# Kernel tuning notes

Hardware: AMD Instinct MI355X
Metric: run time of the kernel (lower is better)

## Reference

```python
import jax, jax.numpy as jnp
import numpy as np

B, S, D, H, F = 2, 2048, 2048, 16, 8192
HD = D // H  # 128
EPS = 1e-5


def setup_inputs() -> dict:
    key = jax.random.key(0)
    ks = jax.random.split(key, 10)
    s = 0.02
    return {
        "x": jax.random.normal(ks[0], (B, S, D), dtype=jnp.float32),
        "rms_w": jnp.ones((D,), dtype=jnp.float32),
        "w_qkv": jax.random.normal(ks[1], (3 * D, D), dtype=jnp.float32) * s,
        "w_out": jax.random.normal(ks[2], (D, D), dtype=jnp.float32) * s,
        "w1": jax.random.normal(ks[3], (F, D), dtype=jnp.float32) * s,
        "b1": jnp.zeros((F,), dtype=jnp.float32),
        "w3": jax.random.normal(ks[4], (F, D), dtype=jnp.float32) * s,
        "b3": jnp.zeros((F,), dtype=jnp.float32),
        "w2": jax.random.normal(ks[5], (D, F), dtype=jnp.float32) * s,
        "b2": jnp.zeros((D,), dtype=jnp.float32),
    }


def reference(x, rms_w, w_qkv, w_out, w1, b1, w3, b3, w2, b2):
    b, s, d = x.shape
    # RMSNorm (computed in fp32 as in original)
    xf = x.astype(jnp.float32)
    xn = (xf * jax.lax.rsqrt(jnp.mean(xf * xf, axis=-1, keepdims=True) + EPS)).astype(x.dtype) * rms_w
    # QKV projection: Linear(dim, 3*dim, bias=False) then 'b n (qkv h d) -> qkv b h n d'
    qkv = jnp.einsum('bsd,ed->bse', xn, w_qkv).reshape(b, s, 3, H, HD)
    qkv = jnp.transpose(qkv, (2, 0, 3, 1, 4))  # [3, b, h, s, hd]
    q, k, v = qkv[0], qkv[1], qkv[2]
    # Naive causal attention with explicit [b,h,s,s] score matrix
    scores = jnp.einsum('bhqd,bhkd->bhqk', q, k) / jnp.sqrt(jnp.float32(HD)).astype(x.dtype)
    causal = jnp.tril(jnp.ones((s, s), dtype=bool))
    scores = jnp.where(causal[None, None], scores, -jnp.inf)
    p = jax.nn.softmax(scores, axis=-1)
    # dropout p=0.0 -> identity
    out = jnp.einsum('bhqk,bhkd->bhqd', p, v)
    # Faithful to original: .view(bs, seqlen, h*d) on [b,h,s,hd] = raw row-major reshape
    out = out.reshape(b, s, H * HD)
    h = out @ w_out.T
    # FeedForward: w2(w1(h) + relu(w3(h))), biases per nn.Linear defaults
    ffn = ((h @ w1.T + b1) + jax.nn.relu(h @ w3.T + b3)) @ w2.T + b2
    return x + ffn
```

## Files before the change

### kernel.cpp

```cpp
#include <hip/hip_runtime.h>
#include <hip/hip_bf16.h>
#include <cstdint>

#define BB 2
#define SS 2048
#define DD 2048
#define HH 16
#define HD 128
#define FF 8192
#define QKVD 6144

typedef __bf16 bf16x8 __attribute__((ext_vector_type(8)));
typedef float floatx4 __attribute__((ext_vector_type(4)));

#define LOG2E 1.4426950408889634f

__device__ __forceinline__ unsigned short f2bf(float f) {
  unsigned u = __builtin_bit_cast(unsigned, f);
  u += 0x7FFFu + ((u >> 16) & 1u);
  return (unsigned short)(u >> 16);
}
__device__ __forceinline__ float bf2f(unsigned short h) {
  return __builtin_bit_cast(float, (unsigned)h << 16);
}

__device__ __forceinline__ void load_lds_16B(const void* g, void* l) {
  __builtin_amdgcn_global_load_lds(
      (const __attribute__((address_space(1))) unsigned int*)g,
      (__attribute__((address_space(3))) unsigned int*)l, 16, 0, 0);
}

__global__ void f32_to_bf16_vec(const float* __restrict__ src,
                                unsigned short* __restrict__ dst, int n4) {
  int i = blockIdx.x * 256 + threadIdx.x;
  if (i < n4) {
    float4 v = ((const float4*)src)[i];
    ushort4 o;
    o.x = f2bf(v.x); o.y = f2bf(v.y); o.z = f2bf(v.z); o.w = f2bf(v.w);
    ((ushort4*)dst)[i] = o;
  }
}

__global__ __launch_bounds__(256) void rmsnorm_bf16(const float* __restrict__ x,
                                                    const float* __restrict__ w,
                                                    unsigned short* __restrict__ xn) {
  const int row = blockIdx.x, tid = threadIdx.x;
  const float4* xr = (const float4*)(x + (size_t)row * DD);
  float4 a = xr[tid], b = xr[tid + 256];
  float ss = a.x * a.x + a.y * a.y + a.z * a.z + a.w * a.w +
             b.x * b.x + b.y * b.y + b.z * b.z + b.w * b.w;
#pragma unroll
  for (int off = 1; off < 64; off <<= 1) ss += __shfl_xor(ss, off);
  __shared__ float red[4];
  if ((tid & 63) == 0) red[tid >> 6] = ss;
  __syncthreads();
  float tot = red[0] + red[1] + red[2] + red[3];
  float sc = rsqrtf(tot * (1.0f / (float)DD) + 1e-5f);
  const float4* wr = (const float4*)w;
  float4 wa = wr[tid], wb = wr[tid + 256];
  ushort4 oa, ob;
  oa.x = f2bf(a.x * sc * wa.x); oa.y = f2bf(a.y * sc * wa.y);
  oa.z = f2bf(a.z * sc * wa.z); oa.w = f2bf(a.w * sc * wa.w);
  ob.x = f2bf(b.x * sc * wb.x); ob.y = f2bf(b.y * sc * wb.y);
  ob.z = f2bf(b.z * sc * wb.z); ob.w = f2bf(b.w * sc * wb.w);
  *(ushort4*)&xn[(size_t)row * DD + tid * 4] = oa;
  *(ushort4*)&xn[(size_t)row * DD + (tid + 256) * 4] = ob;
}

__global__ __launch_bounds__(256) void reduce_wout(const float* __restrict__ p,
                                                   unsigned short* __restrict__ outb,
                                                   int n4) {
  int i = blockIdx.x * 256 + threadIdx.x;
  if (i < n4) {
    float4 a = ((const float4*)p)[i];
    float4 b = ((const float4*)(p + (size_t)BB * SS * DD))[i];
    ushort4 o;
    o.x = f2bf(a.x + b.x); o.y = f2bf(a.y + b.y);
    o.z = f2bf(a.z + b.z); o.w = f2bf(a.w + b.w);
    ((ushort4*)outb)[i] = o;
  }
}

__global__ __launch_bounds__(256) void reduce_w2(const float* __restrict__ p,
                                                 const float* __restrict__ b2,
                                                 const float* __restrict__ x,
                                                 float* __restrict__ out, int n4) {
  int i = blockIdx.x * 256 + threadIdx.x;
  if (i < n4) {
    float4 a = ((const float4*)p)[i];
    float4 b = ((const float4*)(p + (size_t)BB * SS * DD))[i];
    float4 xx = ((const float4*)x)[i];
    float4 bb = ((const float4*)b2)[i & (DD / 4 - 1)];
    float4 o;
    o.x = a.x + b.x + bb.x + xx.x;
    o.y = a.y + b.y + bb.y + xx.y;
    o.z = a.z + b.z + bb.z + xx.z;
    o.w = a.w + b.w + bb.w + xx.w;
    ((float4*)out)[i] = o;
  }
}

template <int MODE>
__global__ __launch_bounds__(512, 1) void gemm_bt(
    const unsigned short* __restrict__ A, const unsigned short* __restrict__ Bw,
    void* __restrict__ Cout, const float* __restrict__ bias,
    const unsigned short* __restrict__ aux, const float* __restrict__ res,
    int M, int N, int K, int lda) {
  __shared__ __align__(16) unsigned short As[2][2][128 * 64];
  __shared__ __align__(16) unsigned short Bs[2][2][128 * 64];
  const int tid = threadIdx.x;
  const int lane = tid & 63, w = tid >> 6;
  const int l16 = lane & 15, quad = lane >> 4;
  const int wm = w >> 2, wn = w & 3;

  const int gx = gridDim.x;
  const int nwg = gx * gridDim.y;
  const int bid = blockIdx.y * gx + blockIdx.x;
  const int cpx = nwg >> 3;
  const int swzb = (bid & 7) * cpx + (bid >> 3);
  const int n0 = (swzb % gx) * 256, m0 = (swzb / gx) * 256;
  const size_t koff = (size_t)blockIdx.z * K;

  const int NT = K >> 6, NIT = NT >> 1;

  const int sr = lane >> 3, sc = lane & 7;
  const unsigned short* pA0 =
      A + (size_t)(m0 + w * 8 + sr) * lda + koff + (sc ^ sr) * 8;
  const unsigned short* pA1 = pA0 + (size_t)128 * lda;
  const unsigned short* pB0 =
      Bw + (size_t)(n0 + (w >> 2) * 64 + (w & 3) * 8 + sr) * lda + koff + (sc ^ sr) * 8;
  const unsigned short* pB1 = pB0 + (size_t)128 * lda;

#define STAGE_A(d, h, kt)                                              \
  {                                                                    \
    const int _k = ((kt) < NT ? (kt) : NT - 1) * 64;                   \
    const size_t _ho = (size_t)(h) * 64 * lda;                         \
    load_lds_16B(pA0 + _ho + _k, &As[d][h][(w * 8) * 64]);             \
    load_lds_16B(pA1 + _ho + _k, &As[d][h][(64 + w * 8) * 64]);        \
  }
#define STAGE_B(d, h, kt)                                              \
  {                                                                    \
    const int _k = ((kt) < NT ? (kt) : NT - 1) * 64;                   \
    const size_t _ho = (size_t)(h) * 32 * lda;                         \
    load_lds_16B(pB0 + _ho + _k, &Bs[d][h][(w * 8) * 64]);             \
    load_lds_16B(pB1 + _ho + _k, &Bs[d][h][(64 + w * 8) * 64]);        \
  }

  floatx4 acc[2][2][4][2];
#pragma unroll
  for (int a0 = 0; a0 < 2; a0++)
#pragma unroll
    for (int a1 = 0; a1 < 2; a1++)
#pragma unroll
      for (int a2 = 0; a2 < 4; a2++)
#pragma unroll
        for (int a3 = 0; a3 < 2; a3++) acc[a0][a1][a2][a3] = floatx4{0.f, 0.f, 0.f, 0.f};
  bf16x8 bb[2][2];

#define PHASE(d, mq, nq, LOADB, STAGES, VMW)                                    \
  {                                                                             \
    bf16x8 a_[4][2];                                                            \
    _Pragma("unroll") for (int fr = 0; fr < 4; ++fr) {                          \
      const int lr_ = wm * 64 + fr * 16 + l16;                                  \
      _Pragma("unroll") for (int kc = 0; kc < 2; ++kc)                          \
        a_[fr][kc] = *(const bf16x8*)&As[d][mq]                                 \
            [lr_ * 64 + (((kc * 4 + quad) ^ (l16 & 7)) * 8)];                   \
    }                                                                           \
    if (LOADB) {                                                                \
      _Pragma("unroll") for (int fn = 0; fn < 2; ++fn) {                        \
        const int lr_ = wn * 32 + fn * 16 + l16;                                \
        _Pragma("unroll") for (int kc = 0; kc < 2; ++kc)                        \
          bb[fn][kc] = *(const bf16x8*)&Bs[d][nq]                               \
              [lr_ * 64 + (((kc * 4 + quad) ^ (l16 & 7)) * 8)];                 \
      }                                                                         \
    }                                                                           \
    STAGES                                                                      \
    __builtin_amdgcn_s_barrier();                                               \
    asm volatile("s_waitcnt lgkmcnt(0)" ::: "memory");                          \
    __builtin_amdgcn_sched_barrier(0);                                          \
    __builtin_amdgcn_s_setprio(1);                                              \
    _Pragma("unroll") for (int kc = 0; kc < 2; ++kc)                            \
      _Pragma("unroll") for (int fr = 0; fr < 4; ++fr)                          \
        _Pragma("unroll") for (int fn = 0; fn < 2; ++fn)                        \
          acc[mq][nq][fr][fn] = __builtin_amdgcn_mfma_f32_16x16x32_bf16(        \
              a_[fr][kc], bb[fn][kc], acc[mq][nq][fr][fn], 0, 0, 0);            \
    __builtin_amdgcn_s_setprio(0);                                              \
    if (VMW) asm volatile("s_waitcnt vmcnt(4)" ::: "memory");                   \
    __builtin_amdgcn_s_barrier();                                               \
    asm volatile("" ::: "memory");                                              \
  }

  STAGE_A(0, 0, 0)
  STAGE_A(0, 1, 0)
  STAGE_B(0, 0, 0)
  STAGE_B(0, 1, 0)
  STAGE_B(1, 0, 1)
  STAGE_A(1, 0, 1)
  asm volatile("s_waitcnt vmcnt(4)" ::: "memory");
  __builtin_amdgcn_s_barrier();
  asm volatile("" ::: "memory");

#pragma unroll 1
  for (int it = 0; it < NIT; ++it) {
    const int t1 = 2 * it + 1, tn0 = 2 * it + 2, tn1 = 2 * it + 3;
    PHASE(0, 0, 0, true,  STAGE_A(1, 1, t1) STAGE_B(1, 1, t1), false)
    PHASE(0, 1, 0, false, , false)
    PHASE(0, 0, 1, true,  STAGE_B(0, 0, tn0), false)
    PHASE(0, 1, 1, false, STAGE_A(0, 0, tn0), true)
    PHASE(1, 0, 0, true,  STAGE_A(0, 1, tn0) STAGE_B(0, 1, tn0), false)
    PHASE(1, 1, 0, false, , false)
    PHASE(1, 0, 1, true,  STAGE_B(1, 0, tn1), false)
    PHASE(1, 1, 1, false, STAGE_A(1, 0, tn1), true)
  }
  asm volatile("s_waitcnt vmcnt(0)" ::: "memory");
#undef PHASE
#undef STAGE_A
#undef STAGE_B

#pragma unroll
  for (int nq = 0; nq < 2; ++nq)
#pragma unroll
    for (int fn = 0; fn < 2; ++fn) {
      const int col = n0 + wn * 64 + nq * 32 + fn * 16 + l16;
      float bv = 0.0f;
      if constexpr (MODE >= 1 && MODE <= 3) bv = bias[col];
#pragma unroll
      for (int mq = 0; mq < 2; ++mq)
#pragma unroll
        for (int fr = 0; fr < 4; ++fr) {
          const int row0 = m0 + wm * 128 + mq * 64 + fr * 16 + quad * 4;
#pragma unroll
          for (int r = 0; r < 4; ++r) {
            const size_t idx = (size_t)(row0 + r) * N + col;
            float v = acc[mq][nq][fr][fn][r];
            if constexpr (MODE == 0) {
              ((unsigned short*)Cout)[idx] = f2bf(v);
            } else if constexpr (MODE == 1) {
              ((unsigned short*)Cout)[idx] = f2bf(v + bv);
            } else if constexpr (MODE == 2) {
              float t = fmaxf(v + bv, 0.0f) + bf2f(aux[idx]);
              ((unsigned short*)Cout)[idx] = f2bf(t);
            } else if constexpr (MODE == 3) {
              ((float*)Cout)[idx] = v + bv + res[idx];
            } else {
              ((float*)Cout)[(size_t)blockIdx.z * ((size_t)M * N) + idx] = v;
            }
          }
        }
    }
}

__global__ __launch_bounds__(256) void attn_fwd(const unsigned short* __restrict__ qkv,
                                                unsigned short* __restrict__ out) {
  __shared__ __align__(16) unsigned short Ks[64 * 136];
  __shared__ __align__(16) unsigned short Vt[128 * 72];
  __shared__ __align__(16) unsigned short Ps[4][32 * 72];
  const int tid = threadIdx.x;
  const int lane = tid & 63, wave = tid >> 6;
  const int l16 = lane & 15, quad = lane >> 4;
  const int p = blockIdx.x, h = blockIdx.y, b = blockIdx.z;
  const float scale = 0.088388347648318447f;

#pragma unroll 1
  for (int pass = 0; pass < 2; pass++) {
    const int qt = pass == 0 ? 15 - p : p;
    const int q0w = qt * 128 + wave * 32;
    const int ntiles = 2 * qt + 2;

    bf16x8 aq[2][4];
#pragma unroll
    for (int mi = 0; mi < 2; mi++) {
      const unsigned short* Qp =
          qkv + (size_t)(b * SS + q0w + mi * 16 + l16) * QKVD + h * HD + quad * 8;
#pragma unroll
      for (int kc = 0; kc < 4; kc++) aq[mi][kc] = *(const bf16x8*)(Qp + kc * 32);
    }

    floatx4 o[2][8];
    float m_r[2][4], l_r[2][4];
#pragma unroll
    for (int mi = 0; mi < 2; mi++) {
#pragma unroll
      for (int nb = 0; nb < 8; nb++) o[mi][nb] = floatx4{0.f, 0.f, 0.f, 0.f};
#pragma unroll
      for (int r = 0; r < 4; r++) { m_r[mi][r] = -1e30f; l_r[mi][r] = 0.f; }
    }

#pragma unroll 1
    for (int t = 0; t < ntiles; t++) {
      const int kv0 = t * 64;
      const bool need_mask = (t >= ntiles - 2);
      __syncthreads();
      {
        const int cc = tid & 15;
#pragma unroll
        for (int i = 0; i < 4; i++) {
          const int r = (tid >> 4) + 16 * i;
          const size_t rowb = (size_t)(b * SS + kv0 + r) * QKVD + h * HD + cc * 8;
          *(uint4*)&Ks[r * 136 + cc * 8] = *(const uint4*)(qkv + rowb + DD);
          unsigned short tmp[8];
          *(uint4*)tmp = *(const uint4*)(qkv + rowb + 2 * DD);
#pragma unroll
          for (int j2 = 0; j2 < 8; j2++) {
            const int d = cc * 8 + j2;
            Vt[d * 72 + (((r >> 3) + (d >> 3)) & 7) * 8 + (r & 7)] = tmp[j2];
          }
        }
      }
      __syncthreads();

      floatx4 s[2][4];
#pragma unroll
      for (int mi = 0; mi < 2; mi++)
#pragma unroll
        for (int ni = 0; ni < 4; ni++) s[mi][ni] = floatx4{0.f, 0.f, 0.f, 0.f};
#pragma unroll
      for (int kc = 0; kc < 4; kc++) {
        bf16x8 bk[4];
#pragma unroll
        for (int ni = 0; ni < 4; ni++)
          bk[ni] = *(const bf16x8*)&Ks[(ni * 16 + l16) * 136 + kc * 32 + quad * 8];
#pragma unroll
        for (int mi = 0; mi < 2; mi++)
#pragma unroll
          for (int ni = 0; ni < 4; ni++)
            s[mi][ni] = __builtin_amdgcn_mfma_f32_16x16x32_bf16(aq[mi][kc], bk[ni],
                                                                s[mi][ni], 0, 0, 0);
      }

#pragma unroll
      for (int mi = 0; mi < 2; mi++) {
        float alpha[4];
#pragma unroll
        for (int r = 0; r < 4; r++) {
          const int qrow = q0w + mi * 16 + quad * 4 + r;
          float v[4];
#pragma unroll
          for (int ni = 0; ni < 4; ni++) {
            v[ni] = s[mi][ni][r] * scale;
            if (need_mask && (kv0 + ni * 16 + l16 > qrow)) v[ni] = -1e30f;
          }
          float mx = fmaxf(fmaxf(v[0], v[1]), fmaxf(v[2], v[3]));
          mx = fmaxf(mx, __shfl_xor(mx, 1));
          mx = fmaxf(mx, __shfl_xor(mx, 2));
          mx = fmaxf(mx, __shfl_xor(mx, 4));
          mx = fmaxf(mx, __shfl_xor(mx, 8));
          const float mnew = fmaxf(m_r[mi][r], mx);
          alpha[r] = exp2f((m_r[mi][r] - mnew) * LOG2E);
          m_r[mi][r] = mnew;
          float rs = 0.f;
#pragma unroll
          for (int ni = 0; ni < 4; ni++) {
            v[ni] = exp2f((v[ni] - mnew) * LOG2E);
            rs += v[ni];
          }
          rs += __shfl_xor(rs, 1);
          rs += __shfl_xor(rs, 2);
          rs += __shfl_xor(rs, 4);
          rs += __shfl_xor(rs, 8);
          l_r[mi][r] = l_r[mi][r] * alpha[r] + rs;
          unsigned short* Pw = &Ps[wave][(mi * 16 + quad * 4 + r) * 72 + l16];
#pragma unroll
          for (int ni = 0; ni < 4; ni++) Pw[ni * 16] = f2bf(v[ni]);
        }
#pragma unroll
        for (int nb = 0; nb < 8; nb++)
#pragma unroll
          for (int r = 0; r < 4; r++) o[mi][nb][r] *= alpha[r];
      }
      asm volatile("s_waitcnt lgkmcnt(0)" ::: "memory");

      bf16x8 pa[2][2];
#pragma unroll
      for (int mi = 0; mi < 2; mi++)
#pragma unroll
        for (int kc2 = 0; kc2 < 2; kc2++)
          pa[mi][kc2] =
              *(const bf16x8*)&Ps[wave][(mi * 16 + l16) * 72 + kc2 * 32 + quad * 8];
#pragma unroll
      for (int nb = 0; nb < 8; nb++) {
        const int d = nb * 16 + l16;
#pragma unroll
        for (int kc2 = 0; kc2 < 2; kc2++) {
          const int chunk = kc2 * 4 + quad;
          bf16x8 bv = *(const bf16x8*)&Vt[d * 72 + ((chunk + (d >> 3)) & 7) * 8];
#pragma unroll
          for (int mi = 0; mi < 2; mi++)
            o[mi][nb] = __builtin_amdgcn_mfma_f32_16x16x32_bf16(pa[mi][kc2], bv,
                                                                o[mi][nb], 0, 0, 0);
        }
      }
    }

#pragma unroll
    for (int mi = 0; mi < 2; mi++) {
      unsigned short* Op =
          out + (size_t)((b * HH + h) * SS + q0w + mi * 16 + quad * 4) * HD + l16;
#pragma unroll
      for (int nb = 0; nb < 8; nb++)
#pragma unroll
        for (int r = 0; r < 4; r++)
          Op[(size_t)r * HD + nb * 16] = f2bf(o[mi][nb][r] / l_r[mi][r]);
    }
  }
}

extern "C" void kernel_launch(void* const* d_in, const int* in_sizes, int n_in,
                              void* d_out, int out_size, void* d_ws, size_t ws_size,
                              hipStream_t stream) {
  const float* x = (const float*)d_in[0];
  const float* rms_w = (const float*)d_in[1];
  const float* w_qkv = (const float*)d_in[2];
  const float* w_out = (const float*)d_in[3];
  const float* w1 = (const float*)d_in[4];
  const float* b1 = (const float*)d_in[5];
  const float* w3 = (const float*)d_in[6];
  const float* b3 = (const float*)d_in[7];
  const float* w2 = (const float*)d_in[8];
  const float* b2 = (const float*)d_in[9];
  float* out = (float*)d_out;

  char* ws = (char*)d_ws;
  size_t off = 0;
  auto alloc = [&](size_t bytes) {
    char* p = ws + off;
    off += (bytes + 255) & ~(size_t)255;
    return p;
  };
  const int M = BB * SS;
  unsigned short* wqkv_b = (unsigned short*)alloc((size_t)QKVD * DD * 2);
  unsigned short* wout_b = (unsigned short*)alloc((size_t)DD * DD * 2);
  unsigned short* w1_b = (unsigned short*)alloc((size_t)FF * DD * 2);
  unsigned short* w3_b = (unsigned short*)alloc((size_t)FF * DD * 2);
  unsigned short* w2_b = (unsigned short*)alloc((size_t)DD * FF * 2);
  unsigned short* xn_b = (unsigned short*)alloc((size_t)M * DD * 2);
  unsigned short* qkv_b = (unsigned short*)alloc((size_t)M * QKVD * 2);
  unsigned short* attn_b = (unsigned short*)alloc((size_t)M * DD * 2);
  unsigned short* h_b = (unsigned short*)alloc((size_t)M * DD * 2);
  unsigned short* act_b = (unsigned short*)alloc((size_t)M * FF * 2);
  float* part = (float*)xn_b;

  f32_to_bf16_vec<<<(QKVD * DD / 4) / 256, 256, 0, stream>>>(w_qkv, wqkv_b, QKVD * DD / 4);
  f32_to_bf16_vec<<<(DD * DD / 4) / 256, 256, 0, stream>>>(w_out, wout_b, DD * DD / 4);
  f32_to_bf16_vec<<<(FF * DD / 4) / 256, 256, 0, stream>>>(w1, w1_b, FF * DD / 4);
  f32_to_bf16_vec<<<(FF * DD / 4) / 256, 256, 0, stream>>>(w3, w3_b, FF * DD / 4);
  f32_to_bf16_vec<<<(DD * FF / 4) / 256, 256, 0, stream>>>(w2, w2_b, DD * FF / 4);

  rmsnorm_bf16<<<M, 256, 0, stream>>>(x, rms_w, xn_b);

  gemm_bt<0><<<dim3(QKVD / 256, M / 256), 512, 0, stream>>>(
      xn_b, wqkv_b, qkv_b, nullptr, nullptr, nullptr, M, QKVD, DD, DD);

  attn_fwd<<<dim3(8, HH, BB), 256, 0, stream>>>(qkv_b, attn_b);

  gemm_bt<4><<<dim3(DD / 256, M / 256, 2), 512, 0, stream>>>(
      attn_b, wout_b, part, nullptr, nullptr, nullptr, M, DD, DD / 2, DD);
  reduce_wout<<<(M * DD / 4) / 256, 256, 0, stream>>>(part, h_b, M * DD / 4);

  gemm_bt<1><<<dim3(FF / 256, M / 256), 512, 0, stream>>>(
      h_b, w1_b, act_b, b1, nullptr, nullptr, M, FF, DD, DD);

  gemm_bt<2><<<dim3(FF / 256, M / 256), 512, 0, stream>>>(
      h_b, w3_b, act_b, b3, act_b, nullptr, M, FF, DD, DD);

  gemm_bt<4><<<dim3(DD / 256, M / 256, 2), 512, 0, stream>>>(
      act_b, w2_b, part, nullptr, nullptr, nullptr, M, DD, FF / 2, FF);
  reduce_w2<<<(M * DD / 4) / 256, 256, 0, stream>>>(part, b2, x, out, M * DD / 4);
}
```

Before: 1.189 ms.

## Pipeline attention K/V loads with double buffering and transposed LDS reads for V

The attention kernel now gives each block a single query tile (grid doubled, with batch-dependent tile order) rather than two passes. K/V tiles are prefetched into registers and double-buffered in LDS so global loads overlap compute. V is stored untransposed and read with ds_read_b64_tr_b16 instead of the scalar scatter transpose, and XOR swizzles replace padding for K and P. The kernel also requests two blocks per CU, which adds LDS and register pressure and relies on hand-placed waitcnt and sched barriers.

```diff
diff --git a/kernel.cpp b/kernel.cpp
--- a/kernel.cpp
+++ b/kernel.cpp
@@ -11,6 +11,7 @@
 #define QKVD 6144
 
 typedef __bf16 bf16x8 __attribute__((ext_vector_type(8)));
+typedef __bf16 bf16x4 __attribute__((ext_vector_type(4)));
 typedef float floatx4 __attribute__((ext_vector_type(4)));
 
 #define LOG2E 1.4426950408889634f
@@ -250,158 +251,213 @@
     }
 }
 
-__global__ __launch_bounds__(256) void attn_fwd(const unsigned short* __restrict__ qkv,
-                                                unsigned short* __restrict__ out) {
-  __shared__ __align__(16) unsigned short Ks[64 * 136];
-  __shared__ __align__(16) unsigned short Vt[128 * 72];
-  __shared__ __align__(16) unsigned short Ps[4][32 * 72];
+__global__ __launch_bounds__(256, 2) void attn_fwd(const unsigned short* __restrict__ qkv,
+                                                   unsigned short* __restrict__ out) {
+  __shared__ __align__(16) unsigned short Ks[2][64 * 128];
+  __shared__ __align__(16) unsigned short Vs[2][64 * 128];
+  __shared__ __align__(16) unsigned short Ps[4][32 * 64];
   const int tid = threadIdx.x;
   const int lane = tid & 63, wave = tid >> 6;
   const int l16 = lane & 15, quad = lane >> 4;
-  const int p = blockIdx.x, h = blockIdx.y, b = blockIdx.z;
+  const int h = blockIdx.y, b = blockIdx.z;
+  const int qt = (b == 0) ? (int)blockIdx.x : 15 - (int)blockIdx.x;
   const float scale = 0.088388347648318447f;
+  const int q0w = qt * 128 + wave * 32;
+  const int ntiles = 2 * qt + 2;
+  const int cc = tid & 15, rr = tid >> 4;
+  const unsigned vbase0 = (unsigned)(size_t)(
+      __attribute__((address_space(3))) unsigned short*)&Vs[0][0];
+
+  bf16x8 aq[2][4];
+#pragma unroll
+  for (int mi = 0; mi < 2; mi++) {
+    const unsigned short* Qp =
+        qkv + (size_t)(b * SS + q0w + mi * 16 + l16) * QKVD + h * HD + quad * 8;
+#pragma unroll
+    for (int kc = 0; kc < 4; kc++) aq[mi][kc] = *(const bf16x8*)(Qp + kc * 32);
+  }
+
+  floatx4 o[2][8];
+  float m_r[2][4], l_r[2][4];
+#pragma unroll
+  for (int mi = 0; mi < 2; mi++) {
+#pragma unroll
+    for (int nb = 0; nb < 8; nb++) o[mi][nb] = floatx4{0.f, 0.f, 0.f, 0.f};
+#pragma unroll
+    for (int r = 0; r < 4; r++) { m_r[mi][r] = -1e30f; l_r[mi][r] = 0.f; }
+  }
+
+  uint4 kreg[4], vreg[4];
+  const unsigned short* kb = qkv + (size_t)b * SS * QKVD + h * HD + cc * 8 + DD;
+
+#define AT_ISSUE(t)                                                           \
+  _Pragma("unroll") for (int i = 0; i < 4; i++) {                             \
+    const size_t rowb = (size_t)((t) * 64 + rr + 16 * i) * QKVD;              \
+    kreg[i] = *(const uint4*)(kb + rowb);                                     \
+    vreg[i] = *(const uint4*)(kb + rowb + DD);                                \
+  }
+#define AT_WRITE(dbuf)                                                        \
+  _Pragma("unroll") for (int i = 0; i < 4; i++) {                             \
+    const int r = rr + 16 * i;                                                \
+    *(uint4*)&Ks[dbuf][r * 128 + ((cc & 8) | ((cc ^ r) & 7)) * 8] = kreg[i];  \
+    *(uint4*)&Vs[dbuf][((r >> 2) * 8 + (cc >> 1)) * 64 + (r & 3) * 16 +       \
+                       (cc & 1) * 8] = vreg[i];                               \
+  }
+#define AT_TRV(o0, o1, o2, o3, addr)                                          \
+  asm volatile("ds_read_b64_tr_b16 %0, %4\n\t"                                \
+               "ds_read_b64_tr_b16 %1, %4 offset:1024\n\t"                    \
+               "ds_read_b64_tr_b16 %2, %4 offset:8192\n\t"                    \
+               "ds_read_b64_tr_b16 %3, %4 offset:9216"                        \
+               : "=&v"(o0), "=&v"(o1), "=&v"(o2), "=&v"(o3)                   \
+               : "v"(addr) : "memory");
+#define AT_MMA(s0, s1, s2, s3, nb, WN)                                        \
+  asm volatile("s_waitcnt lgkmcnt(" WN ")" ::: "memory");                     \
+  __builtin_amdgcn_sched_barrier(0);                                          \
+  {                                                                           \
+    bf16x8 bv0, bv1;                                                          \
+    _Pragma("unroll") for (int j = 0; j < 4; j++) {                           \
+      bv0[j] = s0[j]; bv0[4 + j] = s1[j];                                     \
+      bv1[j] = s2[j]; bv1[4 + j] = s3[j];                                     \
+    }                                                                         \
+    o[0][nb] = __builtin_amdgcn_mfma_f32_16x16x32_bf16(pa[0][0], bv0,         \
+                                                       o[0][nb], 0, 0, 0);    \
+    o[1][nb] = __builtin_amdgcn_mfma_f32_16x16x32_bf16(pa[1][0], bv0,         \
+                                                       o[1][nb], 0, 0, 0);    \
+    o[0][nb] = __builtin_amdgcn_mfma_f32_16x16x32_bf16(pa[0][1], bv1,         \
+                                                       o[0][nb], 0, 0, 0);    \
+    o[1][nb] = __builtin_amdgcn_mfma_f32_16x16x32_bf16(pa[1][1], bv1,         \
+                                                       o[1][nb], 0, 0, 0);    \
+  }
+
+  AT_ISSUE(0)
+  AT_WRITE(0)
+  AT_ISSUE(1)
+  __syncthreads();
 
 #pragma unroll 1
-  for (int pass = 0; pass < 2; pass++) {
-    const int qt = pass == 0 ? 15 - p : p;
-    const int q0w = qt * 128 + wave * 32;
-    const int ntiles = 2 * qt + 2;
-
-    bf16x8 aq[2][4];
+  for (int t = 0; t < ntiles; t++) {
+    const int cur = t & 1;
+    const int kv0 = t * 64;
+    const bool need_mask = (t >= ntiles - 2);
+
+    floatx4 s[2][4];
+#pragma unroll
+    for (int mi = 0; mi < 2; mi++)
+#pragma unroll
+      for (int ni = 0; ni < 4; ni++) s[mi][ni] = floatx4{0.f, 0.f, 0.f, 0.f};
+#pragma unroll
+    for (int kc = 0; kc < 4; kc++) {
+      bf16x8 bk[4];
+#pragma unroll
+      for (int ni = 0; ni < 4; ni++) {
+        const int row = ni * 16 + l16;
+        const int c = kc * 4 + quad;
+        bk[ni] = *(const bf16x8*)&Ks[cur][row * 128 +
+                                          ((c & 8) | ((c ^ row) & 7)) * 8];
+      }
+#pragma unroll
+      for (int mi = 0; mi < 2; mi++)
+#pragma unroll
+        for (int ni = 0; ni < 4; ni++)
+          s[mi][ni] = __builtin_amdgcn_mfma_f32_16x16x32_bf16(aq[mi][kc], bk[ni],
+                                                              s[mi][ni], 0, 0, 0);
+    }
+
 #pragma unroll
     for (int mi = 0; mi < 2; mi++) {
-      const unsigned short* Qp =
-          qkv + (size_t)(b * SS + q0w + mi * 16 + l16) * QKVD + h * HD + quad * 8;
-#pragma unroll
-      for (int kc = 0; kc < 4; kc++) aq[mi][kc] = *(const bf16x8*)(Qp + kc * 32);
+      float alpha[4];
+#pragma unroll
+      for (int r = 0; r < 4; r++) {
+        const int qrow = q0w + mi * 16 + quad * 4 + r;
+        float v[4];
+#pragma unroll
+        for (int ni = 0; ni < 4; ni++) {
+          v[ni] = s[mi][ni][r] * scale;
+          if (need_mask && (kv0 + ni * 16 + l16 > qrow)) v[ni] = -1e30f;
+        }
+        float mx = fmaxf(fmaxf(v[0], v[1]), fmaxf(v[2], v[3]));
+        mx = fmaxf(mx, __shfl_xor(mx, 1));
+        mx = fmaxf(mx, __shfl_xor(mx, 2));
+        mx = fmaxf(mx, __shfl_xor(mx, 4));
+        mx = fmaxf(mx, __shfl_xor(mx, 8));
+        const float mnew = fmaxf(m_r[mi][r], mx);
+        alpha[r] = exp2f((m_r[mi][r] - mnew) * LOG2E);
+        m_r[mi][r] = mnew;
+        float rs = 0.f;
+#pragma unroll
+        for (int ni = 0; ni < 4; ni++) {
+          v[ni] = exp2f((v[ni] - mnew) * LOG2E);
+          rs += v[ni];
+        }
+        rs += __shfl_xor(rs, 1);
+        rs += __shfl_xor(rs, 2);
+        rs += __shfl_xor(rs, 4);
+        rs += __shfl_xor(rs, 8);
+        l_r[mi][r] = l_r[mi][r] * alpha[r] + rs;
+        const int prow = mi * 16 + quad * 4 + r;
+        unsigned short* Pw = &Ps[wave][prow * 64 + (l16 & 7)];
+        const int px = (prow & 7) * 8;
+#pragma unroll
+        for (int ni = 0; ni < 4; ni++)
+          Pw[((ni * 2 + (l16 >> 3)) * 8) ^ px] = f2bf(v[ni]);
+      }
+#pragma unroll
+      for (int nb = 0; nb < 8; nb++)
+#pragma unroll
+        for (int r = 0; r < 4; r++) o[mi][nb][r] *= alpha[r];
     }
-
-    floatx4 o[2][8];
-    float m_r[2][4], l_r[2][4];
-#pragma unroll
-    for (int mi = 0; mi < 2; mi++) {
-#pragma unroll
-      for (int nb = 0; nb < 8; nb++) o[mi][nb] = floatx4{0.f, 0.f, 0.f, 0.f};
-#pragma unroll
-      for (int r = 0; r < 4; r++) { m_r[mi][r] = -1e30f; l_r[mi][r] = 0.f; }
+    asm volatile("s_waitcnt lgkmcnt(0)" ::: "memory");
+
+    bf16x8 pa[2][2];
+#pragma unroll
+    for (int mi = 0; mi < 2; mi++)
+#pragma unroll
+      for (int kc2 = 0; kc2 < 2; kc2++)
+        pa[mi][kc2] = *(const bf16x8*)&Ps[wave][(mi * 16 + l16) * 64 +
+                                                (((kc2 * 4 + quad) ^ (l16 & 7)) * 8)];
+    asm volatile("s_waitcnt lgkmcnt(0)" ::: "memory");
+    __builtin_amdgcn_sched_barrier(0);
+
+    const unsigned va = vbase0 + (unsigned)cur * 16384u + quad * 2048 + l16 * 8;
+    bf16x4 tA0, tA1, tA2, tA3, tB0, tB1, tB2, tB3;
+    AT_TRV(tA0, tA1, tA2, tA3, va)
+    AT_TRV(tB0, tB1, tB2, tB3, va + 128)
+    AT_MMA(tA0, tA1, tA2, tA3, 0, "4")
+    AT_TRV(tA0, tA1, tA2, tA3, va + 256)
+    AT_MMA(tB0, tB1, tB2, tB3, 1, "4")
+    AT_TRV(tB0, tB1, tB2, tB3, va + 384)
+    AT_MMA(tA0, tA1, tA2, tA3, 2, "4")
+    AT_TRV(tA0, tA1, tA2, tA3, va + 512)
+    AT_MMA(tB0, tB1, tB2, tB3, 3, "4")
+    AT_TRV(tB0, tB1, tB2, tB3, va + 640)
+    AT_MMA(tA0, tA1, tA2, tA3, 4, "4")
+    AT_TRV(tA0, tA1, tA2, tA3, va + 768)
+    AT_MMA(tB0, tB1, tB2, tB3, 5, "4")
+    AT_TRV(tB0, tB1, tB2, tB3, va + 896)
+    AT_MMA(tA0, tA1, tA2, tA3, 6, "4")
+    AT_MMA(tB0, tB1, tB2, tB3, 7, "0")
+
+    if (t + 1 < ntiles) {
+      __syncthreads();
+      AT_WRITE(cur ^ 1)
+      if (t + 2 < ntiles) AT_ISSUE(t + 2)
+      __syncthreads();
     }
-
-#pragma unroll 1
-    for (int t = 0; t < ntiles; t++) {
-      const int kv0 = t * 64;
-      const bool need_mask = (t >= ntiles - 2);
-      __syncthreads();
-      {
-        const int cc = tid & 15;
-#pragma unroll
-        for (int i = 0; i < 4; i++) {
-          const int r = (tid >> 4) + 16 * i;
-          const size_t rowb = (size_t)(b * SS + kv0 + r) * QKVD + h * HD + cc * 8;
-          *(uint4*)&Ks[r * 136 + cc * 8] = *(const uint4*)(qkv + rowb + DD);
-          unsigned short tmp[8];
-          *(uint4*)tmp = *(const uint4*)(qkv + rowb + 2 * DD);
-#pragma unroll
-          for (int j2 = 0; j2 < 8; j2++) {
-            const int d = cc * 8 + j2;
-            Vt[d * 72 + (((r >> 3) + (d >> 3)) & 7) * 8 + (r & 7)] = tmp[j2];
-          }
-        }
-      }
-      __syncthreads();
-
-      floatx4 s[2][4];
-#pragma unroll
-      for (int mi = 0; mi < 2; mi++)
-#pragma unroll
-        for (int ni = 0; ni < 4; ni++) s[mi][ni] = floatx4{0.f, 0.f, 0.f, 0.f};
-#pragma unroll
-      for (int kc = 0; kc < 4; kc++) {
-        bf16x8 bk[4];
-#pragma unroll
-        for (int ni = 0; ni < 4; ni++)
-          bk[ni] = *(const bf16x8*)&Ks[(ni * 16 + l16) * 136 + kc * 32 + quad * 8];
-#pragma unroll
-        for (int mi = 0; mi < 2; mi++)
-#pragma unroll
-          for (int ni = 0; ni < 4; ni++)
-            s[mi][ni] = __builtin_amdgcn_mfma_f32_16x16x32_bf16(aq[mi][kc], bk[ni],
-                                                                s[mi][ni], 0, 0, 0);
-      }
-
-#pragma unroll
-      for (int mi = 0; mi < 2; mi++) {
-        float alpha[4];
-#pragma unroll
-        for (int r = 0; r < 4; r++) {
-          const int qrow = q0w + mi * 16 + quad * 4 + r;
-          float v[4];
-#pragma unroll
-          for (int ni = 0; ni < 4; ni++) {
-            v[ni] = s[mi][ni][r] * scale;
-            if (need_mask && (kv0 + ni * 16 + l16 > qrow)) v[ni] = -1e30f;
-          }
-          float mx = fmaxf(fmaxf(v[0], v[1]), fmaxf(v[2], v[3]));
-          mx = fmaxf(mx, __shfl_xor(mx, 1));
-          mx = fmaxf(mx, __shfl_xor(mx, 2));
-          mx = fmaxf(mx, __shfl_xor(mx, 4));
-          mx = fmaxf(mx, __shfl_xor(mx, 8));
-          const float mnew = fmaxf(m_r[mi][r], mx);
-          alpha[r] = exp2f((m_r[mi][r] - mnew) * LOG2E);
-          m_r[mi][r] = mnew;
-          float rs = 0.f;
-#pragma unroll
-          for (int ni = 0; ni < 4; ni++) {
-            v[ni] = exp2f((v[ni] - mnew) * LOG2E);
-            rs += v[ni];
-          }
-          rs += __shfl_xor(rs, 1);
-          rs += __shfl_xor(rs, 2);
-          rs += __shfl_xor(rs, 4);
-          rs += __shfl_xor(rs, 8);
-          l_r[mi][r] = l_r[mi][r] * alpha[r] + rs;
-          unsigned short* Pw = &Ps[wave][(mi * 16 + quad * 4 + r) * 72 + l16];
-#pragma unroll
-          for (int ni = 0; ni < 4; ni++) Pw[ni * 16] = f2bf(v[ni]);
-        }
-#pragma unroll
-        for (int nb = 0; nb < 8; nb++)
-#pragma unroll
-          for (int r = 0; r < 4; r++) o[mi][nb][r] *= alpha[r];
-      }
-      asm volatile("s_waitcnt lgkmcnt(0)" ::: "memory");
-
-      bf16x8 pa[2][2];
-#pragma unroll
-      for (int mi = 0; mi < 2; mi++)
-#pragma unroll
-        for (int kc2 = 0; kc2 < 2; kc2++)
-          pa[mi][kc2] =
-              *(const bf16x8*)&Ps[wave][(mi * 16 + l16) * 72 + kc2 * 32 + quad * 8];
-#pragma unroll
-      for (int nb = 0; nb < 8; nb++) {
-        const int d = nb * 16 + l16;
-#pragma unroll
-        for (int kc2 = 0; kc2 < 2; kc2++) {
-          const int chunk = kc2 * 4 + quad;
-          bf16x8 bv = *(const bf16x8*)&Vt[d * 72 + ((chunk + (d >> 3)) & 7) * 8];
-#pragma unroll
-          for (int mi = 0; mi < 2; mi++)
-            o[mi][nb] = __builtin_amdgcn_mfma_f32_16x16x32_bf16(pa[mi][kc2], bv,
-                                                                o[mi][nb], 0, 0, 0);
-        }
-      }
-    }
-
-#pragma unroll
-    for (int mi = 0; mi < 2; mi++) {
-      unsigned short* Op =
-          out + (size_t)((b * HH + h) * SS + q0w + mi * 16 + quad * 4) * HD + l16;
-#pragma unroll
-      for (int nb = 0; nb < 8; nb++)
-#pragma unroll
-        for (int r = 0; r < 4; r++)
-          Op[(size_t)r * HD + nb * 16] = f2bf(o[mi][nb][r] / l_r[mi][r]);
-    }
+  }
+#undef AT_ISSUE
+#undef AT_WRITE
+#undef AT_TRV
+#undef AT_MMA
+
+#pragma unroll
+  for (int mi = 0; mi < 2; mi++) {
+    unsigned short* Op =
+        out + (size_t)((b * HH + h) * SS + q0w + mi * 16 + quad * 4) * HD + l16;
+#pragma unroll
+    for (int nb = 0; nb < 8; nb++)
+#pragma unroll
+      for (int r = 0; r < 4; r++)
+        Op[(size_t)r * HD + nb * 16] = f2bf(o[mi][nb][r] / l_r[mi][r]);
   }
 }
 
@@ -451,7 +507,7 @@
   gemm_bt<0><<<dim3(QKVD / 256, M / 256), 512, 0, stream>>>(
       xn_b, wqkv_b, qkv_b, nullptr, nullptr, nullptr, M, QKVD, DD, DD);
 
-  attn_fwd<<<dim3(8, HH, BB), 256, 0, stream>>>(qkv_b, attn_b);
+  attn_fwd<<<dim3(16, HH, BB), 256, 0, stream>>>(qkv_b, attn_b);
 
   gemm_bt<4><<<dim3(DD / 256, M / 256, 2), 512, 0, stream>>>(
       attn_b, wout_b, part, nullptr, nullptr, nullptr, M, DD, DD / 2, DD);
```

Measured after the change: 1.141 ms. 1.04x faster.
